# Optimization experiments

Measured on AMD Instinct MI355X. Metric: run time of the kernel, lower is better.

Reference implementation:

```python
import jax, jax.numpy as jnp
import numpy as np

N = 100000
E = 1600000
EMB = 256
D = 128
B = 4096
L = 50
NCLASS = 10


def _spmm(edge_src, edge_dst, edge_w, h):
    # adj @ h with adj given as weighted edge list (dst aggregates from src)
    msg = h[edge_src] * edge_w[:, None]          # [E, D]
    return jax.ops.segment_sum(msg, edge_dst, num_segments=h.shape[0])


def setup_inputs() -> dict:
    key = jax.random.key(0)
    ks = jax.random.split(key, 20)
    inp = {}
    inp["A1_tensor"] = jax.random.normal(ks[0], (N, EMB), dtype=jnp.float32)
    inp["edge_src"] = jax.random.randint(ks[1], (E,), 0, N, dtype=jnp.int32)
    inp["edge_dst"] = jax.random.randint(ks[2], (E,), 0, N, dtype=jnp.int32)
    inp["edge_w"] = jax.random.uniform(ks[3], (E,), dtype=jnp.float32)
    inp["batch_idx"] = jax.random.randint(ks[4], (B, 1, L), 0, N, dtype=jnp.int32)
    s = 0.05  # modest init scale for numerical sanity
    inp["w_gc1"] = jax.random.normal(ks[5], (EMB, D), dtype=jnp.float32) * s
    inp["b_gc1"] = jax.random.normal(ks[6], (D,), dtype=jnp.float32) * s
    inp["w_gc2"] = jax.random.normal(ks[7], (D, D), dtype=jnp.float32) * s
    inp["b_gc2"] = jax.random.normal(ks[8], (D,), dtype=jnp.float32) * s
    inp["n_param"] = jax.random.uniform(ks[9], (N, 1), dtype=jnp.float32)
    inp["Lin1"] = jax.random.normal(ks[10], (EMB, D), dtype=jnp.float32) * s
    inp["Lin1_bias"] = jax.random.normal(ks[11], (D,), dtype=jnp.float32) * s
    inp["weight2"] = jax.random.normal(ks[12], (D, 64), dtype=jnp.float32) * s
    inp["bias2"] = jax.random.normal(ks[13], (64,), dtype=jnp.float32) * s
    inp["lin1_w"] = jax.random.normal(ks[14], ((L + 1) * 64, D), dtype=jnp.float32) * s
    inp["lin1_b"] = jax.random.normal(ks[15], (D,), dtype=jnp.float32) * s
    inp["classifier"] = jax.random.normal(ks[16], (D, NCLASS), dtype=jnp.float32) * s
    inp["classifier_bias"] = jax.random.normal(ks[17], (NCLASS,), dtype=jnp.float32) * s
    return inp


def reference(A1_tensor, edge_src, edge_dst, edge_w, batch_idx,
              w_gc1, b_gc1, w_gc2, b_gc2, n_param, Lin1, Lin1_bias,
              weight2, bias2, lin1_w, lin1_b, classifier, classifier_bias):
    # eval mode: both dropouts are identity
    a0 = A1_tensor @ Lin1 + Lin1_bias              # [N, D]
    a1 = a0 * n_param                              # per-node convex gate
    x1 = _spmm(edge_src, edge_dst, edge_w, A1_tensor @ w_gc1 + b_gc1)  # gc1
    x1 = a1 + x1 * (1.0 - n_param)
    x2 = _spmm(edge_src, edge_dst, edge_w, x1 @ w_gc2 + b_gc2)         # gc2
    bidx = batch_idx[:, 0, :]                      # [B, L]
    sel = x2[bidx]                                 # [B, L, D] irregular gather
    sel = jnp.concatenate([sel, jnp.sum(sel, axis=1, keepdims=True)], axis=1)  # [B, L+1, D]
    sel = jnp.einsum('bld,de->ble', sel, weight2) + bias2                      # [B, L+1, 64]
    sel = sel.reshape(bidx.shape[0], -1)           # [B, (L+1)*64]
    sel = sel @ lin1_w + lin1_b                    # [B, D]
    pre = sel @ classifier + classifier_bias       # [B, nclass]
    return (jnp.argmax(pre, axis=-1), sel)
```

## Files before the change

### kernel.cpp

```cpp
#include <hip/hip_runtime.h>
#include <cstdint>

#define NN   100000
#define EE   1600000
#define EMBD 256
#define DD   128
#define BBB  4096
#define LLL  50
#define NCLS 10

#define NB   196
#define BSH  9
#define EPB  4096

#define FIXS 1048576.0f
#define INVS (1.0f / 1048576.0f)

template<int BM, int BN, int BK, int TM, int TN>
__global__ __launch_bounds__(256)
void gemm_f32(const float* __restrict__ Av, int lda,
              const float* __restrict__ W, int ldw,
              const float* __restrict__ bias,
              float* __restrict__ Cv, int ldc,
              int M, int ktot, int kper,
              const int* __restrict__ bidxg,
              const float* __restrict__ Sg,
              float* __restrict__ Cs)
{
  constexpr int TX = BN / TN;
  constexpr int TY = BM / TM;
  static_assert(TX * TY == 256, "thread mapping");
  static_assert(TN % 4 == 0, "epilogue uses 4-wide vectors");
  constexpr int AQ = BK / 4;
  constexpr int ALOADS = (BM * AQ) / 256;
  static_assert((BM * AQ) % 256 == 0, "A-tile load mapping");
  constexpr int WQ4 = BN / 4;
  constexpr int WLOADS = (BK * WQ4) / 256;
  static_assert((BK * WQ4) % 256 == 0, "W-tile load mapping");

  __shared__ float As[BK][BM + 4];
  __shared__ float Ws[BK][BN];

  const int tid = threadIdx.x;
  const int tx = tid % TX, ty = tid / TX;
  const int bm0 = blockIdx.x * BM;
  const int bn0 = blockIdx.y * BN;
  const int z = blockIdx.z;
  const int koff = z * kper;
  int kc = ktot - koff; if (kc > kper) kc = kper;
  W += bn0 + (size_t)koff * ldw;
  Cv += (Cs == nullptr) ? (size_t)z * (size_t)M * ldc : 0;
  const float* biasp = bias ? bias + bn0 : nullptr;

  float acc[TM][TN];
#pragma unroll
  for (int i = 0; i < TM; ++i)
#pragma unroll
    for (int j = 0; j < TN; ++j) acc[i][j] = 0.f;

  for (int kt = 0; kt < kc; kt += BK) {
#pragma unroll
    for (int p = 0; p < ALOADS; ++p) {
      int f = tid + p * 256;
      int row = f / AQ, q = f % AQ;
      int arow = bm0 + row;
      float4 av = make_float4(0.f, 0.f, 0.f, 0.f);
      if (arow < M) {
        if (bidxg) {
          int k = koff + kt + (q << 2);
          int l = k >> 6, jj = k & 63;
          const float* ap = (l < LLL)
              ? (Av + (size_t)bidxg[arow * LLL + l] * 64 + jj)
              : (Sg + (size_t)arow * 64 + jj);
          av = *(const float4*)ap;
        } else {
          av = *(const float4*)(Av + (long long)arow * lda + koff + kt + (q << 2));
        }
      }
      As[(q << 2) + 0][row] = av.x;
      As[(q << 2) + 1][row] = av.y;
      As[(q << 2) + 2][row] = av.z;
      As[(q << 2) + 3][row] = av.w;
    }
#pragma unroll
    for (int p = 0; p < WLOADS; ++p) {
      int f = tid + p * 256;
      int krow = f / WQ4, c4 = f % WQ4;
      *(float4*)&Ws[krow][c4 << 2] =
          *(const float4*)(W + (long long)(kt + krow) * ldw + (c4 << 2));
    }
    __syncthreads();
#pragma unroll
    for (int kk = 0; kk < BK; ++kk) {
      float a[TM], b[TN];
      if constexpr (TM % 4 == 0) {
#pragma unroll
        for (int i = 0; i < TM; i += 4)
          *(float4*)&a[i] = *(const float4*)&As[kk][ty * TM + i];
      } else {
#pragma unroll
        for (int i = 0; i < TM; ++i) a[i] = As[kk][ty * TM + i];
      }
#pragma unroll
      for (int j = 0; j < TN; j += 4)
        *(float4*)&b[j] = *(const float4*)&Ws[kk][tx * TN + j];
#pragma unroll
      for (int i = 0; i < TM; ++i)
#pragma unroll
        for (int j = 0; j < TN; ++j)
          acc[i][j] = fmaf(a[i], b[j], acc[i][j]);
    }
    __syncthreads();
  }

#pragma unroll
  for (int i = 0; i < TM; ++i) {
    int r = bm0 + ty * TM + i;
    if (r >= M) continue;
#pragma unroll
    for (int j4 = 0; j4 < TN; j4 += 4) {
      float4 v = make_float4(acc[i][j4], acc[i][j4 + 1],
                             acc[i][j4 + 2], acc[i][j4 + 3]);
      if (biasp != nullptr) {
        v.x += biasp[tx * TN + j4 + 0]; v.y += biasp[tx * TN + j4 + 1];
        v.z += biasp[tx * TN + j4 + 2]; v.w += biasp[tx * TN + j4 + 3];
      }
      int col = bn0 + tx * TN + j4;
      float* cp;
      if (Cs != nullptr)
        cp = (col < 64) ? (Cv + (long long)r * 64 + col)
                        : (Cs + (long long)r * 64 + (col - 64));
      else
        cp = Cv + (long long)r * ldc + col;
      *(float4*)cp = v;
    }
  }
}

__global__ __launch_bounds__(256)
void fuse1_k(const float* __restrict__ wgc1, const float* __restrict__ lin1,
             const float* __restrict__ bgc1, const float* __restrict__ lin1b,
             const float* __restrict__ wgc2,
             float* __restrict__ T1, float* __restrict__ T2,
             float* __restrict__ ta, float* __restrict__ tb)
{
  int t = blockIdx.x * 256 + threadIdx.x;
  const float* Arow; float* outp; int n;
  if (t < 32768)      { n = t & 127; Arow = wgc1 + (t >> 7) * 128; outp = T1 + t; }
  else if (t < 65536) { int u = t - 32768; n = u & 127; Arow = lin1 + (u >> 7) * 128; outp = T2 + u; }
  else if (t < 65664) { n = t - 65536; Arow = bgc1;  outp = ta + n; }
  else if (t < 65792) { n = t - 65664; Arow = lin1b; outp = tb + n; }
  else return;
  float s = 0.f;
  for (int k = 0; k < 128; ++k) s = fmaf(Arow[k], wgc2[k * 128 + n], s);
  *outp = s;
}

__global__ __launch_bounds__(256)
void fuse2_k(const float* __restrict__ T1, const float* __restrict__ T2,
             const float* __restrict__ ta, const float* __restrict__ tb,
             const float* __restrict__ bgc2, const float* __restrict__ w2,
             float* __restrict__ Wab, float* __restrict__ bab,
             float* __restrict__ bcv)
{
  int t = blockIdx.x * 256 + threadIdx.x;
  const float* Arow; float* outp; int j;
  if (t < 32768) {
    int c = t & 127; j = c & 63;
    Arow = (c < 64 ? T1 : T2) + (t >> 7) * 128;
    outp = Wab + t;
  } else if (t < 32896) {
    int c = t - 32768; j = c & 63; Arow = (c < 64) ? ta : tb; outp = bab + c;
  } else if (t < 32960) {
    j = t - 32896; Arow = bgc2; outp = bcv + j;
  } else return;
  float s = 0.f;
  for (int k = 0; k < 128; ++k) s = fmaf(Arow[k], w2[k * 64 + j], s);
  *outp = s;
}

__global__ __launch_bounds__(256)
void cnt_k(const int* __restrict__ edst, int* __restrict__ gbkt)
{
  __shared__ int l[NB];
  const int tid = threadIdx.x;
  for (int i = tid; i < NB; i += 256) l[i] = 0;
  __syncthreads();
  const int e0 = blockIdx.x * EPB;
  const int e1 = min(EE, e0 + EPB);
#pragma unroll
  for (int u = 0; u < 16; ++u) {
    int e = e0 + u * 256 + tid;
    if (e < e1) atomicAdd(&l[edst[e] >> BSH], 1);
  }
  __syncthreads();
  for (int i = tid; i < NB; i += 256)
    if (l[i]) atomicAdd(&gbkt[i], l[i]);
}

__global__ __launch_bounds__(256)
void scanB_k(const int* __restrict__ gbkt, int* __restrict__ bbase,
             int* __restrict__ gcur, int* __restrict__ rp)
{
  __shared__ int s[256];
  int t = threadIdx.x;
  int v = (t < NB) ? gbkt[t] : 0;
  s[t] = v;
  __syncthreads();
  for (int off = 1; off < 256; off <<= 1) {
    int u = (t >= off) ? s[t - off] : 0;
    __syncthreads();
    s[t] += u;
    __syncthreads();
  }
  if (t < NB) {
    int ex = s[t] - v;
    bbase[t] = ex;
    gcur[t] = ex;
  }
  if (t == 0) { bbase[NB] = EE; rp[NN] = EE; }
}

__global__ __launch_bounds__(256)
void bin_k(const int* __restrict__ edst, const int* __restrict__ esrc,
           const float* __restrict__ ew, int* __restrict__ gcur,
           int4* __restrict__ ebd)
{
  __shared__ int lcnt[NB];
  __shared__ int lbase[NB];
  const int tid = threadIdx.x;
  const int e0 = blockIdx.x * EPB;
  const int e1 = min(EE, e0 + EPB);
  for (int i = tid; i < NB; i += 256) lcnt[i] = 0;
  __syncthreads();
  int dv[16], sv[16], wv[16];
#pragma unroll
  for (int u = 0; u < 16; ++u) {
    int e = e0 + u * 256 + tid;
    if (e < e1) {
      dv[u] = edst[e];
      sv[u] = esrc[e];
      wv[u] = __float_as_int(ew[e]);
      atomicAdd(&lcnt[dv[u] >> BSH], 1);
    } else dv[u] = -1;
  }
  __syncthreads();
  for (int i = tid; i < NB; i += 256) {
    lbase[i] = atomicAdd(&gcur[i], lcnt[i]);
    lcnt[i] = 0;
  }
  __syncthreads();
#pragma unroll
  for (int u = 0; u < 16; ++u) {
    if (dv[u] >= 0) {
      int c = dv[u] >> BSH;
      int k = atomicAdd(&lcnt[c], 1);
      int4 p; p.x = dv[u]; p.y = sv[u]; p.z = wv[u]; p.w = 0;
      ebd[lbase[c] + k] = p;
    }
  }
}

__global__ __launch_bounds__(256)
void sort_k(const int4* __restrict__ ebd, const int* __restrict__ bbase,
            int* __restrict__ rp, int2* __restrict__ sw)
{
  __shared__ int hist[512];
  __shared__ int excl[512];
  __shared__ int s2[256];
  __shared__ int lcur[512];
  const int c = blockIdx.x;
  const int n0 = c << BSH;
  const int n1 = min(NN, n0 + 512);
  const int nn = n1 - n0;
  const int tid = threadIdx.x;
  for (int i = tid; i < 512; i += 256) { hist[i] = 0; lcur[i] = 0; }
  __syncthreads();
  const int b0 = bbase[c];
  const int b1 = bbase[c + 1];
  for (int i = b0 + tid; i < b1; i += 256)
    atomicAdd(&hist[ebd[i].x - n0], 1);
  __syncthreads();
  int a0 = hist[2 * tid], a1 = hist[2 * tid + 1];
  s2[tid] = a0 + a1;
  __syncthreads();
  for (int off = 1; off < 256; off <<= 1) {
    int u = (tid >= off) ? s2[tid - off] : 0;
    __syncthreads();
    s2[tid] += u;
    __syncthreads();
  }
  int pe = tid ? s2[tid - 1] : 0;
  excl[2 * tid] = pe;
  excl[2 * tid + 1] = pe + a0;
  if (2 * tid < nn)     rp[n0 + 2 * tid]     = b0 + pe;
  if (2 * tid + 1 < nn) rp[n0 + 2 * tid + 1] = b0 + pe + a0;
  __syncthreads();
  for (int i = b0 + tid; i < b1; i += 256) {
    int4 p = ebd[i];
    int li = p.x - n0;
    int k = atomicAdd(&lcur[li], 1);
    int2 q; q.x = p.y; q.y = p.z;
    sw[b0 + excl[li] + k] = q;
  }
}

template<int MODE>
__global__ __launch_bounds__(256)
void spmm64(const int* __restrict__ rp, const int2* __restrict__ sw,
            const float* __restrict__ Gf, float* __restrict__ xout,
            const float* __restrict__ bias, const float* __restrict__ npar,
            const float* __restrict__ Pb)
{
  int widx = blockIdx.x * 4 + (threadIdx.x >> 6);
  if (widx >= NN) return;
  int lane = threadIdx.x & 63;
  int e0 = rp[widx], e1 = rp[widx + 1];
  int acc = 0;
  int j = e0;
  for (; j + 8 <= e1; j += 8) {
    float gv[8], wv[8];
#pragma unroll
    for (int u = 0; u < 8; ++u) {
      int2 q = sw[j + u];
      wv[u] = __int_as_float(q.y);
      gv[u] = Gf[(size_t)q.x * 64 + lane];
    }
#pragma unroll
    for (int u = 0; u < 8; ++u)
      acc += __float2int_rn(gv[u] * wv[u] * FIXS);
  }
  for (; j < e1; ++j) {
    int2 q = sw[j];
    acc += __float2int_rn(Gf[(size_t)q.x * 64 + lane] *
                          __int_as_float(q.y) * FIXS);
  }
  float v = (float)acc * INVS;
  if (MODE == 1) {
    xout[(size_t)widx * 64 + lane] = v + bias[lane];
  } else {
    float nv = npar[widx];
    float p = Pb[(size_t)widx * 64 + lane];
    xout[(size_t)widx * 64 + lane] = nv * p + (1.f - nv) * v + bias[lane];
  }
}

__global__ __launch_bounds__(256)
void sumS_k(const float* __restrict__ Z, const int* __restrict__ bidx,
            const float* __restrict__ b2, float* __restrict__ S)
{
  int wv = threadIdx.x >> 6;
  int lane = threadIdx.x & 63;
  int b = blockIdx.x * 4 + wv;
  if (b >= BBB) return;
  const int* bi = bidx + (size_t)b * LLL;
  float s = 0.f;
  for (int l = 0; l < LLL; ++l)
    s += Z[(size_t)bi[l] * 64 + lane];
  S[(size_t)b * 64 + lane] = s - 49.f * b2[lane];
}

__global__ __launch_bounds__(256)
void reduce4_k(const float* __restrict__ P4, const float* __restrict__ l1b,
               float* __restrict__ sel)
{
  int t = blockIdx.x * 256 + threadIdx.x;
  if (t >= BBB * 32) return;
  int r = t >> 5, c4 = t & 31;
  size_t off = (size_t)r * 128 + (c4 << 2);
  const size_t zs = (size_t)BBB * 128;
  float4 s0 = *(const float4*)(P4 + off);
  float4 s1 = *(const float4*)(P4 + zs + off);
  float4 s2 = *(const float4*)(P4 + 2 * zs + off);
  float4 s3 = *(const float4*)(P4 + 3 * zs + off);
  float4 b  = *(const float4*)(l1b + (c4 << 2));
  float4 o;
  o.x = ((s0.x + s1.x) + s2.x) + s3.x + b.x;
  o.y = ((s0.y + s1.y) + s2.y) + s3.y + b.y;
  o.z = ((s0.z + s1.z) + s2.z) + s3.z + b.z;
  o.w = ((s0.w + s1.w) + s2.w) + s3.w + b.w;
  *(float4*)(sel + off) = o;
}

__global__ __launch_bounds__(256)
void cls_k(const float* __restrict__ sel, const float* __restrict__ Wc,
           const float* __restrict__ bc, float* __restrict__ outIdx)
{
  int wv = threadIdx.x >> 6;
  int lane = threadIdx.x & 63;
  int b = blockIdx.x * 4 + wv;
  if (b >= BBB) return;
  float logit = -1e30f;
  if (lane < NCLS) {
    float s = bc[lane];
    const float* sr = sel + (size_t)b * DD;
    for (int d = 0; d < DD; ++d) s = fmaf(sr[d], Wc[d * NCLS + lane], s);
    logit = s;
  }
  float best = -1e30f; int bi = 0;
  for (int c = 0; c < NCLS; ++c) {
    float v = __shfl(logit, c, 64);
    if (v > best) { best = v; bi = c; }
  }
  if (lane == 0) outIdx[b] = (float)bi;
}

extern "C" void kernel_launch(void* const* d_in, const int* in_sizes, int n_in,
                              void* d_out, int out_size, void* d_ws, size_t ws_size,
                              hipStream_t stream)
{
  const float* A1    = (const float*)d_in[0];
  const int*   esrc  = (const int*)d_in[1];
  const int*   edst  = (const int*)d_in[2];
  const float* ew    = (const float*)d_in[3];
  const int*   bidx  = (const int*)d_in[4];
  const float* wgc1  = (const float*)d_in[5];
  const float* bgc1  = (const float*)d_in[6];
  const float* wgc2  = (const float*)d_in[7];
  const float* bgc2  = (const float*)d_in[8];
  const float* npar  = (const float*)d_in[9];
  const float* lin1  = (const float*)d_in[10];
  const float* lin1b = (const float*)d_in[11];
  const float* w2    = (const float*)d_in[12];
  const float* b2    = (const float*)d_in[13];
  const float* l1w   = (const float*)d_in[14];
  const float* l1b   = (const float*)d_in[15];
  const float* clsw  = (const float*)d_in[16];
  const float* clsb  = (const float*)d_in[17];

  float* out = (float*)d_out;
  float* sel = out + BBB;

  uint8_t* ws   = (uint8_t*)d_ws;
  int4*    ebd  = (int4*) (ws);
  float*   Qb   = (float*)(ws);
  float*   Z    = (float*)(ws);
  float*   Pb   = (float*)(ws + 25600000);
  float*   G    = (float*)(ws + 51200000);
  float*   P4   = (float*)(ws + 51200000);
  int2*    sw   = (int2*) (ws + 76800000);
  int*     rp   = (int*)  (ws + 89600000);
  int*     gbkt = (int*)  (ws + 90000016);
  int*     gcur = (int*)  (ws + 90001040);
  int*     bbase= (int*)  (ws + 90002064);
  float*   S    = (float*)(ws + 90400528);
  float*   T1   = (float*)(ws + 91449104);
  float*   T2   = (float*)(ws + 91580176);
  float*   Wab  = (float*)(ws + 91711248);
  float*   ta   = (float*)(ws + 91842320);
  float*   tb   = (float*)(ws + 91842832);
  float*   bab  = (float*)(ws + 91843344);
  float*   bcv  = (float*)(ws + 91843856);

  dim3 blk(256);
  const int gEB = (EE + EPB - 1) / EPB;

  hipLaunchKernelGGL(fuse1_k, dim3(257), blk, 0, stream,
      wgc1, lin1, bgc1, lin1b, wgc2, T1, T2, ta, tb);
  hipLaunchKernelGGL(fuse2_k, dim3(129), blk, 0, stream,
      T1, T2, ta, tb, bgc2, w2, Wab, bab, bcv);

  hipMemsetAsync(gbkt, 0, NB * 4, stream);
  hipLaunchKernelGGL(cnt_k, dim3(gEB), blk, 0, stream, edst, gbkt);
  hipLaunchKernelGGL(scanB_k, dim3(1), blk, 0, stream, gbkt, bbase, gcur, rp);
  hipLaunchKernelGGL(bin_k, dim3(gEB), blk, 0, stream, edst, esrc, ew, gcur, ebd);
  hipLaunchKernelGGL(sort_k, dim3(NB), blk, 0, stream, ebd, bbase, rp, sw);

  hipLaunchKernelGGL((gemm_f32<64,128,32,8,4>), dim3(1563, 1, 1), blk, 0, stream,
      A1, EMBD, Wab, 128, bab, Qb, 64,
      NN, EMBD, EMBD, (const int*)nullptr, (const float*)nullptr, Pb);

  hipLaunchKernelGGL((spmm64<2>), dim3(NN / 4), blk, 0, stream,
      rp, sw, Qb, G, bcv, npar, Pb);

  hipLaunchKernelGGL((spmm64<1>), dim3(NN / 4), blk, 0, stream,
      rp, sw, G, Z, b2, (const float*)nullptr, (const float*)nullptr);

  hipLaunchKernelGGL(sumS_k, dim3(BBB / 4), blk, 0, stream, Z, bidx, b2, S);

  hipLaunchKernelGGL((gemm_f32<32,64,32,2,4>), dim3(BBB / 32, 2, 4), blk, 0, stream,
      Z, 64, l1w, DD, (const float*)nullptr, P4, DD,
      BBB, (LLL + 1) * 64, 13 * 64, bidx, S, (float*)nullptr);

  hipLaunchKernelGGL(reduce4_k, dim3(BBB * 32 / 256), blk, 0, stream, P4, l1b, sel);

  hipLaunchKernelGGL(cls_k, dim3(BBB / 4), blk, 0, stream, sel, clsw, clsb, out);
}
```

Before: 418.5 us.

## Replace fp32 node GEMM with split-bf16 MFMA kernel

The large N×256×128 projection GEMM moves from a scalar fp32 tiled kernel to an MFMA kernel. Each fp32 value is split into high and low bf16 parts, and three bf16 MFMAs (hh, hl, lh) recover near-fp32 accuracy. A small prep kernel converts the fused weight matrix into pre-swizzled hi/lo bf16 fragments, and the generic GEMM loses its split-output path. The aim is to cut compute time on the dense GEMM, at the cost of a slight accuracy loss from dropping the lo*lo term and some extra conversion work.

```diff
diff --git a/kernel.cpp b/kernel.cpp
--- a/kernel.cpp
+++ b/kernel.cpp
@@ -16,6 +16,18 @@
 #define FIXS 1048576.0f
 #define INVS (1.0f / 1048576.0f)
 
+typedef __attribute__((ext_vector_type(8))) short bf16x8;
+typedef __attribute__((ext_vector_type(4))) float f32x4;
+
+__device__ __forceinline__ ushort f2bf(float f) {
+  uint32_t u = __float_as_uint(f);
+  u += 0x7fffu + ((u >> 16) & 1u);
+  return (ushort)(u >> 16);
+}
+__device__ __forceinline__ float bf2f(ushort h) {
+  return __uint_as_float(((uint32_t)h) << 16);
+}
+
 template<int BM, int BN, int BK, int TM, int TN>
 __global__ __launch_bounds__(256)
 void gemm_f32(const float* __restrict__ Av, int lda,
@@ -24,8 +36,7 @@
               float* __restrict__ Cv, int ldc,
               int M, int ktot, int kper,
               const int* __restrict__ bidxg,
-              const float* __restrict__ Sg,
-              float* __restrict__ Cs)
+              const float* __restrict__ Sg)
 {
   constexpr int TX = BN / TN;
   constexpr int TY = BM / TM;
@@ -49,7 +60,7 @@
   const int koff = z * kper;
   int kc = ktot - koff; if (kc > kper) kc = kper;
   W += bn0 + (size_t)koff * ldw;
-  Cv += (Cs == nullptr) ? (size_t)z * (size_t)M * ldc : 0;
+  Cv += (size_t)z * (size_t)M * ldc;
   const float* biasp = bias ? bias + bn0 : nullptr;
 
   float acc[TM][TN];
@@ -125,16 +136,102 @@
         v.x += biasp[tx * TN + j4 + 0]; v.y += biasp[tx * TN + j4 + 1];
         v.z += biasp[tx * TN + j4 + 2]; v.w += biasp[tx * TN + j4 + 3];
       }
-      int col = bn0 + tx * TN + j4;
-      float* cp;
-      if (Cs != nullptr)
-        cp = (col < 64) ? (Cv + (long long)r * 64 + col)
-                        : (Cs + (long long)r * 64 + (col - 64));
-      else
-        cp = Cv + (long long)r * ldc + col;
-      *(float4*)cp = v;
-    }
-  }
+      *(float4*)(Cv + (long long)r * ldc + bn0 + tx * TN + j4) = v;
+    }
+  }
+}
+
+__global__ __launch_bounds__(256)
+void gemm_qp_mfma(const float* __restrict__ A1,
+                  const ushort* __restrict__ Wfh,
+                  const ushort* __restrict__ Wfl,
+                  const float* __restrict__ bab,
+                  float* __restrict__ Qb, float* __restrict__ Pb, int M)
+{
+  __shared__ ushort LAh[64][32];
+  __shared__ ushort LAl[64][32];
+  const int tid = threadIdx.x;
+  const int w = tid >> 6, l = tid & 63;
+  const int bm0 = blockIdx.x * 64;
+  const int srow = tid >> 2, skg = tid & 3;
+  const int frow = (w << 4) + (l & 15);
+  const int fk   = (l >> 4) << 3;
+
+  f32x4 acc[8];
+#pragma unroll
+  for (int c = 0; c < 8; ++c) acc[c] = (f32x4){0.f, 0.f, 0.f, 0.f};
+
+  for (int kt8 = 0; kt8 < 8; ++kt8) {
+    {
+      int grow = bm0 + srow;
+      float x[8];
+      if (grow < M) {
+        const float* ap = A1 + (size_t)grow * 256 + (kt8 << 5) + (skg << 3);
+        *(float4*)&x[0] = *(const float4*)ap;
+        *(float4*)&x[4] = *(const float4*)(ap + 4);
+      } else {
+#pragma unroll
+        for (int j = 0; j < 8; ++j) x[j] = 0.f;
+      }
+      ushort h[8], lo[8];
+#pragma unroll
+      for (int j = 0; j < 8; ++j) {
+        h[j] = f2bf(x[j]);
+        lo[j] = f2bf(x[j] - bf2f(h[j]));
+      }
+      *(bf16x8*)&LAh[srow][skg << 3] = *(bf16x8*)h;
+      *(bf16x8*)&LAl[srow][skg << 3] = *(bf16x8*)lo;
+    }
+    __syncthreads();
+
+    bf16x8 ah = *(const bf16x8*)&LAh[frow][fk];
+    bf16x8 al = *(const bf16x8*)&LAl[frow][fk];
+#pragma unroll
+    for (int ct = 0; ct < 8; ++ct) {
+      size_t off = ((size_t)((kt8 << 3) + ct) * 64 + l) << 3;
+      bf16x8 bh = *(const bf16x8*)(Wfh + off);
+      bf16x8 bl = *(const bf16x8*)(Wfl + off);
+      acc[ct] = __builtin_amdgcn_mfma_f32_16x16x32_bf16(ah, bh, acc[ct], 0, 0, 0);
+      acc[ct] = __builtin_amdgcn_mfma_f32_16x16x32_bf16(ah, bl, acc[ct], 0, 0, 0);
+      acc[ct] = __builtin_amdgcn_mfma_f32_16x16x32_bf16(al, bh, acc[ct], 0, 0, 0);
+    }
+    __syncthreads();
+  }
+
+  const int r0 = bm0 + (w << 4) + ((l >> 4) << 2);
+#pragma unroll
+  for (int ct = 0; ct < 8; ++ct) {
+    int gcol = (ct << 4) + (l & 15);
+    float bia = bab[gcol];
+    float* dst = (gcol < 64) ? (Qb + gcol) : (Pb + (gcol - 64));
+#pragma unroll
+    for (int r = 0; r < 4; ++r) {
+      int grow = r0 + r;
+      if (grow < M) dst[(size_t)grow * 64] = acc[ct][r] + bia;
+    }
+  }
+}
+
+__global__ __launch_bounds__(256)
+void wfrag_k(const float* __restrict__ Wab, ushort* __restrict__ Wfh,
+             ushort* __restrict__ Wfl)
+{
+  int t = blockIdx.x * 256 + threadIdx.x;
+  if (t >= 4096) return;
+  int f = t >> 6, l = t & 63;
+  int kt = f >> 3, ct = f & 7;
+  int row0 = (kt << 5) + ((l >> 4) << 3);
+  int col = (ct << 4) + (l & 15);
+  ushort h[8], lo[8];
+#pragma unroll
+  for (int j = 0; j < 8; ++j) {
+    float x = Wab[(row0 + j) * 128 + col];
+    h[j] = f2bf(x);
+    lo[j] = f2bf(x - bf2f(h[j]));
+  }
+  size_t off = ((size_t)t) << 3;
+  *(bf16x8*)(Wfh + off) = *(bf16x8*)h;
+  *(bf16x8*)(Wfl + off) = *(bf16x8*)lo;
 }
 
 __global__ __launch_bounds__(256)
@@ -451,6 +548,8 @@
   float*   tb   = (float*)(ws + 91842832);
   float*   bab  = (float*)(ws + 91843344);
   float*   bcv  = (float*)(ws + 91843856);
+  ushort*  Wfh  = (ushort*)(ws + 91844112);
+  ushort*  Wfl  = (ushort*)(ws + 91909648);
 
   dim3 blk(256);
   const int gEB = (EE + EPB - 1) / EPB;
@@ -459,6 +558,7 @@
       wgc1, lin1, bgc1, lin1b, wgc2, T1, T2, ta, tb);
   hipLaunchKernelGGL(fuse2_k, dim3(129), blk, 0, stream,
       T1, T2, ta, tb, bgc2, w2, Wab, bab, bcv);
+  hipLaunchKernelGGL(wfrag_k, dim3(16), blk, 0, stream, Wab, Wfh, Wfl);
 
   hipMemsetAsync(gbkt, 0, NB * 4, stream);
   hipLaunchKernelGGL(cnt_k, dim3(gEB), blk, 0, stream, edst, gbkt);
@@ -466,9 +566,8 @@
   hipLaunchKernelGGL(bin_k, dim3(gEB), blk, 0, stream, edst, esrc, ew, gcur, ebd);
   hipLaunchKernelGGL(sort_k, dim3(NB), blk, 0, stream, ebd, bbase, rp, sw);
 
-  hipLaunchKernelGGL((gemm_f32<64,128,32,8,4>), dim3(1563, 1, 1), blk, 0, stream,
-      A1, EMBD, Wab, 128, bab, Qb, 64,
-      NN, EMBD, EMBD, (const int*)nullptr, (const float*)nullptr, Pb);
+  hipLaunchKernelGGL(gemm_qp_mfma, dim3(1563), blk, 0, stream,
+      A1, Wfh, Wfl, bab, Qb, Pb, NN);
 
   hipLaunchKernelGGL((spmm64<2>), dim3(NN / 4), blk, 0, stream,
       rp, sw, Qb, G, bcv, npar, Pb);
@@ -480,7 +579,7 @@
 
   hipLaunchKernelGGL((gemm_f32<32,64,32,2,4>), dim3(BBB / 32, 2, 4), blk, 0, stream,
       Z, 64, l1w, DD, (const float*)nullptr, P4, DD,
-      BBB, (LLL + 1) * 64, 13 * 64, bidx, S, (float*)nullptr);
+      BBB, (LLL + 1) * 64, 13 * 64, bidx, S);
 
   hipLaunchKernelGGL(reduce4_k, dim3(BBB * 32 / 256), blk, 0, stream, P4, l1b, sel);
 
```

After: 376.7 us. -10.0%, faster.
